# Optimization experiments

Hardware: AMD Instinct MI355X
Metric: run time of the kernel (lower is better)

## Reference

```python
import jax, jax.numpy as jnp
import numpy as np

D, H, L, P, NQ, B, DFF = 256, 8, 4, 4, 900, 4, 1024
SHAPES = [(128, 128), (64, 64), (32, 32), (16, 16)]
S = sum(h * w for h, w in SHAPES)  # 21760
HD = D // H


def setup_inputs() -> dict:
    key = jax.random.key(0)
    ks = iter(jax.random.split(key, 32))
    r = lambda sh, s=1.0: jax.random.normal(next(ks), sh, jnp.float32) * s
    return dict(
        tgt=r((B, NQ, D)),
        query_pos=r((B, NQ, D)),
        reference_points=jax.random.uniform(next(ks), (B, NQ, L, 2), jnp.float32),
        memory=r((B, S, D)),
        in_proj_w=r((D, 3 * D), 0.02), in_proj_b=jnp.zeros(3 * D, jnp.float32),
        out_proj_w=r((D, D), 0.02), out_proj_b=jnp.zeros(D, jnp.float32),
        ln1_g=jnp.ones(D, jnp.float32), ln1_b=jnp.zeros(D, jnp.float32),
        ln2_g=jnp.ones(D, jnp.float32), ln2_b=jnp.zeros(D, jnp.float32),
        ln3_g=jnp.ones(D, jnp.float32), ln3_b=jnp.zeros(D, jnp.float32),
        vproj_w=r((D, D), 0.02), vproj_b=jnp.zeros(D, jnp.float32),
        off_w=r((D, H * L * P * 2), 0.02), off_b=r((H * L * P * 2,), 0.5),
        aw_w=r((D, H * L * P), 0.02), aw_b=jnp.zeros(H * L * P, jnp.float32),
        oproj_w=r((D, D), 0.02), oproj_b=jnp.zeros(D, jnp.float32),
        lin1_w=r((D, DFF), 0.02), lin1_b=jnp.zeros(DFF, jnp.float32),
        lin2_w=r((DFF, D), 0.02), lin2_b=jnp.zeros(D, jnp.float32),
        spatial_shapes=np.array(SHAPES, np.int32),
        mem_mask=jnp.zeros((B, S), bool),
    )


def _ln(x, g, b):
    m = jnp.mean(x, -1, keepdims=True)
    v = jnp.mean((x - m) ** 2, -1, keepdims=True)
    return (x - m) * jax.lax.rsqrt(v + 1e-5) * g + b


def reference(tgt, query_pos, reference_points, memory,
              in_proj_w, in_proj_b, out_proj_w, out_proj_b,
              ln1_g, ln1_b, ln2_g, ln2_b, ln3_g, ln3_b,
              vproj_w, vproj_b, off_w, off_b, aw_w, aw_b, oproj_w, oproj_b,
              lin1_w, lin1_b, lin2_w, lin2_b, spatial_shapes, mem_mask):
    shapes = np.asarray(spatial_shapes)  # static level shapes

    # ---- self attention (nn.MultiheadAttention, q=k=tgt+pos, v=tgt) ----
    qp = tgt + query_pos
    q = qp @ in_proj_w[:, :D] + in_proj_b[:D]
    k = qp @ in_proj_w[:, D:2 * D] + in_proj_b[D:2 * D]
    v = tgt @ in_proj_w[:, 2 * D:] + in_proj_b[2 * D:]
    split = lambda x: x.reshape(B, NQ, H, HD).transpose(0, 2, 1, 3)
    qh, kh, vh = split(q), split(k), split(v)
    att = jax.nn.softmax(jnp.einsum('bhqd,bhkd->bhqk', qh, kh) / np.sqrt(HD).astype(np.float32), -1)
    sa = jnp.einsum('bhqk,bhkd->bhqd', att, vh).transpose(0, 2, 1, 3).reshape(B, NQ, D)
    tgt = _ln(tgt + sa @ out_proj_w + out_proj_b, ln2_g, ln2_b)

    # ---- MSDeformAttn cross attention ----
    query = tgt + query_pos
    value = memory @ vproj_w + vproj_b
    value = jnp.where(mem_mask[..., None], 0.0, value).reshape(B, S, H, HD)
    off = (query @ off_w + off_b).reshape(B, NQ, H, L, P, 2)
    aw = jax.nn.softmax((query @ aw_w + aw_b).reshape(B, NQ, H, L * P), -1).reshape(B, NQ, H, L, P)
    # offset normalizer is (W_l, H_l)
    normalizer = jnp.stack([jnp.asarray(shapes[:, 1]), jnp.asarray(shapes[:, 0])], -1).astype(jnp.float32)
    loc = reference_points[:, :, None, :, None, :] + off / normalizer[None, None, None, :, None, :]

    acc = jnp.zeros((B, NQ, H, HD), tgt.dtype)
    start = 0
    bidx = jnp.arange(B)[:, None, None, None]
    hidx = jnp.arange(H)[None, None, :, None]
    for l in range(L):
        Hl, Wl = int(shapes[l, 0]), int(shapes[l, 1])
        vf = value[:, start:start + Hl * Wl]  # [B, Hl*Wl, H, HD]
        # grid_sample align_corners=False, zero padding: pixel = loc*size - 0.5
        x = loc[:, :, :, l, :, 0] * Wl - 0.5  # [B,NQ,H,P]
        y = loc[:, :, :, l, :, 1] * Hl - 0.5
        x0 = jnp.floor(x); y0 = jnp.floor(y)
        wx = x - x0; wy = y - y0
        x0i = x0.astype(jnp.int32); y0i = y0.astype(jnp.int32)

        def gather(xi, yi):
            valid = (xi >= 0) & (xi < Wl) & (yi >= 0) & (yi < Hl)
            idx = jnp.clip(yi, 0, Hl - 1) * Wl + jnp.clip(xi, 0, Wl - 1)
            g = vf[bidx, idx, hidx]  # [B,NQ,H,P,HD]
            return jnp.where(valid[..., None], g, 0.0)

        samp = (gather(x0i, y0i) * ((1 - wx) * (1 - wy))[..., None]
                + gather(x0i + 1, y0i) * (wx * (1 - wy))[..., None]
                + gather(x0i, y0i + 1) * ((1 - wx) * wy)[..., None]
                + gather(x0i + 1, y0i + 1) * (wx * wy)[..., None])
        acc = acc + (samp * aw[:, :, :, l, :, None]).sum(3)
        start += Hl * Wl

    ca = acc.reshape(B, NQ, D) @ oproj_w + oproj_b
    tgt = _ln(tgt + ca, ln1_g, ln1_b)

    # ---- FFN ----
    ff = jax.nn.relu(tgt @ lin1_w + lin1_b) @ lin2_w + lin2_b
    return _ln(tgt + ff, ln3_g, ln3_b)
```

## Files before the change

### kernel.cpp

```cpp
#include <hip/hip_runtime.h>
#include <hip/hip_bf16.h>

typedef __attribute__((ext_vector_type(8))) short bf16x8;
typedef __attribute__((ext_vector_type(4))) short bf16x4;
typedef __attribute__((ext_vector_type(4))) float f32x4;

#define DEV static __device__ __forceinline__

constexpr int Bc = 4, NQc = 900, Hc = 8, Sc = 21760;
constexpr int M1 = Bc * NQc;
constexpr int NQT = (NQc + 63) / 64;

DEV short f2bf(float f) {
  union { __hip_bfloat16 h; short s; } u;
  u.h = __float2bfloat16(f);
  return u.s;
}
DEV float bf2f(short s) {
  union { short s; __hip_bfloat16 h; } u;
  u.s = s;
  return __bfloat162float(u.h);
}

DEV void pack_body(const float* W, short* Wt, int K, int N, int t) {
  int kq = K >> 2;
  int n = t / kq;
  int k4 = (t - n * kq) * 4;
  bf16x4 o;
  o[0] = f2bf(W[(size_t)(k4 + 0) * N + n]);
  o[1] = f2bf(W[(size_t)(k4 + 1) * N + n]);
  o[2] = f2bf(W[(size_t)(k4 + 2) * N + n]);
  o[3] = f2bf(W[(size_t)(k4 + 3) * N + n]);
  *(bf16x4*)&Wt[((size_t)(k4 >> 5) * N + n) * 32 + (k4 & 31)] = o;
}

__global__ __launch_bounds__(256) void pack_all_k(
    const float* w0, short* t0,
    const float* w1, short* t1,
    const float* w2, short* t2,
    const float* w3, short* t3,
    const float* w4, short* t4,
    const float* w5, short* t5) {
  int t = blockIdx.x * 256 + threadIdx.x;
  if (t < 49152) pack_body(w0, t0, 256, 768, t);
  else if (t < 65536) pack_body(w1, t1, 256, 256, t - 49152);
  else if (t < 81920) pack_body(w2, t2, 256, 256, t - 65536);
  else if (t < 98304) pack_body(w3, t3, 256, 256, t - 81920);
  else if (t < 163840) pack_body(w4, t4, 256, 1024, t - 98304);
  else pack_body(w5, t5, 1024, 256, t - 163840);
}

template <int MODE, int ACT>
__global__ __launch_bounds__(256) void gemmv_k(
    const float* __restrict__ A, const float* __restrict__ A2,
    const short* __restrict__ Wt, const float* __restrict__ bias,
    void* __restrict__ Cv, float* __restrict__ C2, int M, int N, int K,
    const unsigned char* __restrict__ rowmask, const float* __restrict__ g,
    const float* __restrict__ beta, const float* __restrict__ resid,
    const float* __restrict__ qpos, float* __restrict__ out2) {
  __shared__ short As[64 * 40];
  __shared__ short Ws[256 * 40];
  const int nb = N >> 8;
  const int mb = blockIdx.x / nb, bn = blockIdx.x - mb * nb;
  const int tid = threadIdx.x;
  const int lane = tid & 63, wave = tid >> 6;
  const int l16 = lane & 15, quad = lane >> 4;
  const int sr = tid >> 2, sk = (tid & 3) * 8;
  const int arow = mb * 64 + sr;
  const bool aval = arow < M;
  const bool useA2 = (MODE == 2) ? (bn < 2) : (A2 != nullptr);
  const float* ap = A + (size_t)arow * K + sk;
  const float* ap2 = A2 ? A2 + (size_t)arow * K + sk : A;
  const short* wp = Wt + (size_t)(bn * 256 + tid) * 32;
  const size_t wstep = (size_t)N * 32;

  f32x4 acc[4][4] = {};
  float4 a0, a1;
  bf16x8 w0, w1, w2, w3;

  if (aval) {
    a0 = *(const float4*)ap;
    a1 = *(const float4*)(ap + 4);
    if (useA2) {
      float4 b0 = *(const float4*)ap2, b1 = *(const float4*)(ap2 + 4);
      a0.x += b0.x; a0.y += b0.y; a0.z += b0.z; a0.w += b0.w;
      a1.x += b1.x; a1.y += b1.y; a1.z += b1.z; a1.w += b1.w;
    }
  } else {
    a0 = make_float4(0.f, 0.f, 0.f, 0.f);
    a1 = a0;
  }
  w0 = *(const bf16x8*)(wp + 0);
  w1 = *(const bf16x8*)(wp + 8);
  w2 = *(const bf16x8*)(wp + 16);
  w3 = *(const bf16x8*)(wp + 24);

  const int KT = K >> 5;
  for (int it = 0; it < KT; ++it) {
    {
      bf16x8 t;
      t[0] = f2bf(a0.x); t[1] = f2bf(a0.y); t[2] = f2bf(a0.z); t[3] = f2bf(a0.w);
      t[4] = f2bf(a1.x); t[5] = f2bf(a1.y); t[6] = f2bf(a1.z); t[7] = f2bf(a1.w);
      *(bf16x8*)&As[sr * 40 + sk] = t;
    }
    short* wd = &Ws[tid * 40];
    *(bf16x8*)(wd + 0) = w0;
    *(bf16x8*)(wd + 8) = w1;
    *(bf16x8*)(wd + 16) = w2;
    *(bf16x8*)(wd + 24) = w3;
    __syncthreads();
    if (it + 1 < KT) {
      const float* an = ap + (it + 1) * 32;
      if (aval) {
        a0 = *(const float4*)an;
        a1 = *(const float4*)(an + 4);
        if (useA2) {
          const float* an2 = ap2 + (it + 1) * 32;
          float4 b0 = *(const float4*)an2, b1 = *(const float4*)(an2 + 4);
          a0.x += b0.x; a0.y += b0.y; a0.z += b0.z; a0.w += b0.w;
          a1.x += b1.x; a1.y += b1.y; a1.z += b1.z; a1.w += b1.w;
        }
      }
      const short* wn = wp + (it + 1) * wstep;
      w0 = *(const bf16x8*)(wn + 0);
      w1 = *(const bf16x8*)(wn + 8);
      w2 = *(const bf16x8*)(wn + 16);
      w3 = *(const bf16x8*)(wn + 24);
    }
    bf16x8 af[4], bf[4];
#pragma unroll
    for (int i = 0; i < 4; i++)
      af[i] = *(const bf16x8*)&As[(i * 16 + l16) * 40 + quad * 8];
#pragma unroll
    for (int j = 0; j < 4; j++)
      bf[j] = *(const bf16x8*)&Ws[(wave * 64 + j * 16 + l16) * 40 + quad * 8];
#pragma unroll
    for (int i = 0; i < 4; i++)
#pragma unroll
      for (int j = 0; j < 4; j++)
        acc[i][j] = __builtin_amdgcn_mfma_f32_16x16x32_bf16(af[i], bf[j], acc[i][j], 0, 0, 0);
    __syncthreads();
  }

  if (MODE == 2) {
    const bool isqk = (bn < 2);
    float* dst = isqk ? (float*)Cv : C2;
    const int stride = isqk ? 512 : 256;
    const int cb = isqk ? bn * 256 : 0;
#pragma unroll
    for (int i = 0; i < 4; i++)
#pragma unroll
      for (int j = 0; j < 4; j++) {
        const int cl = wave * 64 + j * 16 + l16;
        const float bb = bias[bn * 256 + cl];
#pragma unroll
        for (int r = 0; r < 4; r++) {
          const int m = mb * 64 + i * 16 + quad * 4 + r;
          if (m < M) dst[(size_t)m * stride + cb + cl] = acc[i][j][r] + bb;
        }
      }
  } else if (MODE == 1) {
#pragma unroll
    for (int i = 0; i < 4; i++)
#pragma unroll
      for (int j = 0; j < 4; j++) {
        const int cl = wave * 64 + j * 16 + l16;
        const float bb = bias[cl];
#pragma unroll
        for (int r = 0; r < 4; r++) {
          const int m = mb * 64 + i * 16 + quad * 4 + r;
          if (m < M) {
            float v = acc[i][j][r] + bb;
            if (rowmask[m]) v = 0.f;
            ((short*)Cv)[(size_t)m * 256 + cl] = f2bf(v);
          }
        }
      }
  } else if (MODE == 0) {
#pragma unroll
    for (int i = 0; i < 4; i++)
#pragma unroll
      for (int j = 0; j < 4; j++) {
        const int cl = wave * 64 + j * 16 + l16;
        const int col = bn * 256 + cl;
        const float bb = bias[col];
#pragma unroll
        for (int r = 0; r < 4; r++) {
          const int m = mb * 64 + i * 16 + quad * 4 + r;
          if (m < M) {
            float v = acc[i][j][r] + bb;
            if (ACT == 1) v = fmaxf(v, 0.f);
            ((float*)Cv)[(size_t)m * N + col] = v;
          }
        }
      }
  } else {
#pragma unroll
    for (int j = 0; j < 4; j++) {
      const int cl = wave * 64 + j * 16 + l16;
      const float bb = bias[cl];
#pragma unroll
      for (int i = 0; i < 4; i++)
#pragma unroll
        for (int r = 0; r < 4; r++) {
          const int m = mb * 64 + i * 16 + quad * 4 + r;
          const float rs = (m < M) ? resid[(size_t)m * 256 + cl] : 0.f;
          acc[i][j][r] += bb + rs;
        }
    }
    float2* pr = (float2*)As;
#pragma unroll
    for (int i = 0; i < 4; i++)
#pragma unroll
      for (int r = 0; r < 4; r++) {
        float s = 0.f, q = 0.f;
#pragma unroll
        for (int j = 0; j < 4; j++) {
          s += acc[i][j][r];
          q += acc[i][j][r] * acc[i][j][r];
        }
#pragma unroll
        for (int d = 1; d < 16; d <<= 1) {
          s += __shfl_xor(s, d);
          q += __shfl_xor(q, d);
        }
        if (l16 == 0) pr[(i * 16 + quad * 4 + r) * 4 + wave] = make_float2(s, q);
      }
    __syncthreads();
#pragma unroll
    for (int i = 0; i < 4; i++)
#pragma unroll
      for (int r = 0; r < 4; r++) {
        const int ml = i * 16 + quad * 4 + r;
        float2 p0 = pr[ml * 4 + 0], p1 = pr[ml * 4 + 1];
        float2 p2 = pr[ml * 4 + 2], p3 = pr[ml * 4 + 3];
        const float sum = p0.x + p1.x + p2.x + p3.x;
        const float sq = p0.y + p1.y + p2.y + p3.y;
        const float mean = sum * (1.f / 256.f);
        const float var = sq * (1.f / 256.f) - mean * mean;
        const float rstd = rsqrtf(var + 1e-5f);
        const int m = mb * 64 + ml;
        if (m < M) {
#pragma unroll
          for (int j = 0; j < 4; j++) {
            const int cl = wave * 64 + j * 16 + l16;
            const float o = (acc[i][j][r] - mean) * rstd * g[cl] + beta[cl];
            ((float*)Cv)[(size_t)m * 256 + cl] = o;
            if (out2) out2[(size_t)m * 256 + cl] = o + qpos[(size_t)m * 256 + cl];
          }
        }
      }
  }
}

DEV void gemm32_body(const float* __restrict__ A, const float* __restrict__ W,
                     const float* __restrict__ bias, float* __restrict__ C,
                     int M, int N, int K, int bid) {
  __shared__ float Asf[16][64];
  __shared__ float Bsf[16][68];
  const int nb = N >> 6;
  const int bm = bid / nb, bn = bid % nb;
  const int tid = threadIdx.x;
  const int tm = tid >> 4, tn = tid & 15;
  float acc[4][4] = {};

  for (int k0 = 0; k0 < K; k0 += 16) {
    {
      const int m = tid >> 2, kk = (tid & 3) * 4;
      const int row = bm * 64 + m;
      float4 v = (row < M) ? *(const float4*)(A + (size_t)row * K + k0 + kk)
                           : make_float4(0.f, 0.f, 0.f, 0.f);
      Asf[kk + 0][m] = v.x; Asf[kk + 1][m] = v.y;
      Asf[kk + 2][m] = v.z; Asf[kk + 3][m] = v.w;
    }
    {
      const int kk = tid >> 4, n = (tid & 15) * 4;
      float4 v = *(const float4*)(W + (size_t)(k0 + kk) * N + bn * 64 + n);
      *(float4*)&Bsf[kk][n] = v;
    }
    __syncthreads();
#pragma unroll
    for (int kk = 0; kk < 16; kk++) {
      float a[4], b[4];
#pragma unroll
      for (int i = 0; i < 4; i++) a[i] = Asf[kk][tm * 4 + i];
#pragma unroll
      for (int j = 0; j < 4; j++) b[j] = Bsf[kk][tn * 4 + j];
#pragma unroll
      for (int i = 0; i < 4; i++)
#pragma unroll
        for (int j = 0; j < 4; j++) acc[i][j] = fmaf(a[i], b[j], acc[i][j]);
    }
    __syncthreads();
  }
#pragma unroll
  for (int i = 0; i < 4; i++) {
    const int row = bm * 64 + tm * 4 + i;
    if (row >= M) continue;
#pragma unroll
    for (int j = 0; j < 4; j++) {
      const int col = bn * 64 + tn * 4 + j;
      C[(size_t)row * N + col] = acc[i][j] + bias[col];
    }
  }
}

__global__ __launch_bounds__(256) void gemm32_offaw_k(
    const float* __restrict__ query, const float* __restrict__ off_w,
    const float* __restrict__ off_b, float* __restrict__ offb,
    const float* __restrict__ aw_w, const float* __restrict__ aw_b,
    float* __restrict__ awlin) {
  if (blockIdx.x < 228)
    gemm32_body(query, off_w, off_b, offb, M1, 256, 256, blockIdx.x);
  else
    gemm32_body(query, aw_w, aw_b, awlin, M1, 128, 256, blockIdx.x - 228);
}

__global__ __launch_bounds__(256) void attn_k(const float* __restrict__ qk,
                                              const float* __restrict__ vbuf,
                                              float* __restrict__ sa) {
  __shared__ short Vt[32 * 72];
  __shared__ short Pb[4][16 * 72];
  const int bid = blockIdx.x;
  const int qt = bid % NQT, bh = bid / NQT;
  const int b = bh >> 3, h = bh & 7;
  const int tid = threadIdx.x, lane = tid & 63, wave = tid >> 6;
  const int l16 = lane & 15, quad = lane >> 4;

  const int q_local = qt * 64 + wave * 16 + l16;
  const int qrow = b * NQc + min(q_local, NQc - 1);
  const float scale = 0.17677669529663687f;
  bf16x8 qf;
  {
    const float* qp = qk + (size_t)qrow * 512 + h * 32 + quad * 8;
    float4 v0 = *(const float4*)qp, v1 = *(const float4*)(qp + 4);
    qf[0] = f2bf(v0.x * scale); qf[1] = f2bf(v0.y * scale);
    qf[2] = f2bf(v0.z * scale); qf[3] = f2bf(v0.w * scale);
    qf[4] = f2bf(v1.x * scale); qf[5] = f2bf(v1.y * scale);
    qf[6] = f2bf(v1.z * scale); qf[7] = f2bf(v1.w * scale);
  }
  f32x4 o0 = {}, o1 = {};
  float mrun[4] = {-1e30f, -1e30f, -1e30f, -1e30f};
  float lrun[4] = {0.f, 0.f, 0.f, 0.f};

  for (int kt = 0; kt < NQT; kt++) {
    const int k0 = kt * 64;
    __syncthreads();
#pragma unroll
    for (int i = 0; i < 8; i++) {
      int kk = i * 8 + (tid >> 5);
      int ch = tid & 31;
      int key = k0 + kk;
      float v = (key < NQc) ? vbuf[(size_t)(b * NQc + key) * 256 + h * 32 + ch] : 0.f;
      Vt[ch * 72 + kk] = f2bf(v);
    }
    __syncthreads();

    f32x4 s[4];
#pragma unroll
    for (int st = 0; st < 4; st++) {
      const int key = k0 + st * 16 + l16;
      const int krow = b * NQc + min(key, NQc - 1);
      const float* kp = qk + (size_t)krow * 512 + 256 + h * 32 + quad * 8;
      float4 v0 = *(const float4*)kp, v1 = *(const float4*)(kp + 4);
      bf16x8 kf;
      kf[0] = f2bf(v0.x); kf[1] = f2bf(v0.y); kf[2] = f2bf(v0.z); kf[3] = f2bf(v0.w);
      kf[4] = f2bf(v1.x); kf[5] = f2bf(v1.y); kf[6] = f2bf(v1.z); kf[7] = f2bf(v1.w);
      f32x4 z = {};
      s[st] = __builtin_amdgcn_mfma_f32_16x16x32_bf16(qf, kf, z, 0, 0, 0);
      if (key >= NQc) { s[st][0] = -1e30f; s[st][1] = -1e30f; s[st][2] = -1e30f; s[st][3] = -1e30f; }
    }
    float mnew[4], alpha[4];
#pragma unroll
    for (int r = 0; r < 4; r++) {
      float mx = fmaxf(fmaxf(s[0][r], s[1][r]), fmaxf(s[2][r], s[3][r]));
#pragma unroll
      for (int d = 1; d < 16; d <<= 1) mx = fmaxf(mx, __shfl_xor(mx, d));
      mnew[r] = fmaxf(mrun[r], mx);
      alpha[r] = __expf(mrun[r] - mnew[r]);
      mrun[r] = mnew[r];
    }
    float tsum[4] = {0.f, 0.f, 0.f, 0.f};
#pragma unroll
    for (int st = 0; st < 4; st++) {
#pragma unroll
      for (int r = 0; r < 4; r++) {
        float p = __expf(s[st][r] - mnew[r]);
        s[st][r] = p;
        tsum[r] += p;
      }
    }
#pragma unroll
    for (int r = 0; r < 4; r++) {
      float t = tsum[r];
#pragma unroll
      for (int d = 1; d < 16; d <<= 1) t += __shfl_xor(t, d);
      lrun[r] = lrun[r] * alpha[r] + t;
      o0[r] *= alpha[r];
      o1[r] *= alpha[r];
    }
    short* pw = Pb[wave];
#pragma unroll
    for (int st = 0; st < 4; st++)
#pragma unroll
      for (int r = 0; r < 4; r++)
        pw[(quad * 4 + r) * 72 + st * 16 + l16] = f2bf(s[st][r]);
#pragma unroll
    for (int c = 0; c < 2; c++) {
      bf16x8 pf = *(const bf16x8*)&pw[l16 * 72 + c * 32 + quad * 8];
      bf16x8 vf0 = *(const bf16x8*)&Vt[l16 * 72 + c * 32 + quad * 8];
      bf16x8 vf1 = *(const bf16x8*)&Vt[(16 + l16) * 72 + c * 32 + quad * 8];
      o0 = __builtin_amdgcn_mfma_f32_16x16x32_bf16(pf, vf0, o0, 0, 0, 0);
      o1 = __builtin_amdgcn_mfma_f32_16x16x32_bf16(pf, vf1, o1, 0, 0, 0);
    }
  }
#pragma unroll
  for (int r = 0; r < 4; r++) {
    const int q = qt * 64 + wave * 16 + quad * 4 + r;
    if (q < NQc) {
      const float inv = 1.f / lrun[r];
      sa[(size_t)(b * NQc + q) * 256 + h * 32 + l16] = o0[r] * inv;
      sa[(size_t)(b * NQc + q) * 256 + h * 32 + 16 + l16] = o1[r] * inv;
    }
  }
}

__global__ __launch_bounds__(256) void sample_k(
    const float* __restrict__ awlin, const float* __restrict__ off,
    const float* __restrict__ refp, const short* __restrict__ value,
    float* __restrict__ accout) {
  const int wid = blockIdx.x * 4 + (threadIdx.x >> 6);
  const int lane = threadIdx.x & 63;
  const int bq = wid >> 3, h = wid & 7;
  const int b = bq / NQc;
  const int l16 = lane & 15;

  float wraw = awlin[(size_t)bq * 128 + h * 16 + l16];
  float mx = wraw;
#pragma unroll
  for (int d = 1; d < 16; d <<= 1) mx = fmaxf(mx, __shfl_xor(mx, d));
  float e = __expf(wraw - mx), ssum = e;
#pragma unroll
  for (int d = 1; d < 16; d <<= 1) ssum += __shfl_xor(ssum, d);
  const float wnorm = e / ssum;

  const int ch = lane & 31, sub = lane >> 5;
  float facc = 0.f;
#pragma unroll
  for (int it = 0; it < 8; it++) {
    const int pt = it * 2 + sub;
    const float w = __shfl(wnorm, pt);
    const int l = pt >> 2;
    const int W = 128 >> l;
    const int start = (l == 0) ? 0 : (l == 1) ? 16384 : (l == 2) ? 20480 : 21504;
    const float offx = off[(size_t)bq * 256 + h * 32 + pt * 2];
    const float offy = off[(size_t)bq * 256 + h * 32 + pt * 2 + 1];
    const float rx = refp[(size_t)bq * 8 + l * 2];
    const float ry = refp[(size_t)bq * 8 + l * 2 + 1];
    const float x = rx * (float)W + offx - 0.5f;
    const float y = ry * (float)W + offy - 0.5f;
    const float x0f = floorf(x), y0f = floorf(y);
    const float wx = x - x0f, wy = y - y0f;
    const int x0 = (int)x0f, y0 = (int)y0f;
    const short* vb = value + ((size_t)b * Sc + start) * 256 + h * 32 + ch;
#pragma unroll
    for (int c4 = 0; c4 < 4; c4++) {
      const int dx = c4 & 1, dy = c4 >> 1;
      const int xi = x0 + dx, yi = y0 + dy;
      const bool valid = (xi >= 0) && (xi < W) && (yi >= 0) && (yi < W);
      const int xc = min(max(xi, 0), W - 1);
      const int yc = min(max(yi, 0), W - 1);
      const float gvv = bf2f(vb[(size_t)(yc * W + xc) * 256]);
      const float ww = (dx ? wx : 1.f - wx) * (dy ? wy : 1.f - wy);
      facc += valid ? w * ww * gvv : 0.f;
    }
  }
  facc += __shfl_xor(facc, 32);
  if (lane < 32) accout[(size_t)bq * 256 + h * 32 + ch] = facc;
}

extern "C" void kernel_launch(void* const* d_in, const int* in_sizes, int n_in,
                              void* d_out, int out_size, void* d_ws,
                              size_t ws_size, hipStream_t stream) {
  const float* tgt = (const float*)d_in[0];
  const float* query_pos = (const float*)d_in[1];
  const float* refp = (const float*)d_in[2];
  const float* memory = (const float*)d_in[3];
  const float* in_proj_w = (const float*)d_in[4];
  const float* in_proj_b = (const float*)d_in[5];
  const float* out_proj_w = (const float*)d_in[6];
  const float* out_proj_b = (const float*)d_in[7];
  const float* ln1_g = (const float*)d_in[8];
  const float* ln1_b = (const float*)d_in[9];
  const float* ln2_g = (const float*)d_in[10];
  const float* ln2_b = (const float*)d_in[11];
  const float* ln3_g = (const float*)d_in[12];
  const float* ln3_b = (const float*)d_in[13];
  const float* vproj_w = (const float*)d_in[14];
  const float* vproj_b = (const float*)d_in[15];
  const float* off_w = (const float*)d_in[16];
  const float* off_b = (const float*)d_in[17];
  const float* aw_w = (const float*)d_in[18];
  const float* aw_b = (const float*)d_in[19];
  const float* oproj_w = (const float*)d_in[20];
  const float* oproj_b = (const float*)d_in[21];
  const float* lin1_w = (const float*)d_in[22];
  const float* lin1_b = (const float*)d_in[23];
  const float* lin2_w = (const float*)d_in[24];
  const float* lin2_b = (const float*)d_in[25];
  const unsigned char* mem_mask = (const unsigned char*)d_in[27];
  float* out = (float*)d_out;

  float* ws = (float*)d_ws;
  float* qkbuf = ws + 921600;
  float* vbuf = ws + 2764800;
  float* sa = ws + 3686400;
  float* tgt2 = ws + 5529600;
  float* query = ws + 6451200;
  float* offb = ws + 7372800;
  float* awlin = ws + 8294400;
  float* accb = ws + 8755200;
  float* tgt3 = ws + 9676800;
  float* ff1 = ws + 10598400;
  short* valueBf = (short*)(ws + 14284800);
  short* wbase = valueBf + 22282240;
  short* inT = wbase + 0;
  short* outT = wbase + 196608;
  short* vT = wbase + 262144;
  short* oT = wbase + 327680;
  short* lin1T = wbase + 393216;
  short* lin2T = wbase + 655360;

  pack_all_k<<<896, 256, 0, stream>>>(in_proj_w, inT, out_proj_w, outT,
                                      vproj_w, vT, oproj_w, oT,
                                      lin1_w, lin1T, lin2_w, lin2T);

  gemmv_k<2, 0><<<57 * 3, 256, 0, stream>>>(
      tgt, query_pos, inT, in_proj_b, qkbuf, vbuf, M1, 768, 256,
      nullptr, nullptr, nullptr, nullptr, nullptr, nullptr);
  attn_k<<<Bc * Hc * NQT, 256, 0, stream>>>(qkbuf, vbuf, sa);
  gemmv_k<3, 0><<<57, 256, 0, stream>>>(
      sa, nullptr, outT, out_proj_b, tgt2, nullptr, M1, 256, 256,
      nullptr, ln2_g, ln2_b, tgt, query_pos, query);
  gemmv_k<1, 0><<<1360, 256, 0, stream>>>(
      memory, nullptr, vT, vproj_b, valueBf, nullptr, Bc * Sc, 256, 256,
      mem_mask, nullptr, nullptr, nullptr, nullptr, nullptr);
  gemm32_offaw_k<<<342, 256, 0, stream>>>(query, off_w, off_b, offb, aw_w, aw_b, awlin);
  sample_k<<<Bc * NQc * Hc / 4, 256, 0, stream>>>(awlin, offb, refp, valueBf, accb);
  gemmv_k<3, 0><<<57, 256, 0, stream>>>(
      accb, nullptr, oT, oproj_b, tgt3, nullptr, M1, 256, 256,
      nullptr, ln1_g, ln1_b, tgt2, nullptr, nullptr);
  gemmv_k<0, 1><<<57 * 4, 256, 0, stream>>>(
      tgt3, nullptr, lin1T, lin1_b, ff1, nullptr, M1, 1024, 256,
      nullptr, nullptr, nullptr, nullptr, nullptr, nullptr);
  gemmv_k<3, 0><<<57, 256, 0, stream>>>(
      ff1, nullptr, lin2T, lin2_b, out, nullptr, M1, 256, 1024,
      nullptr, ln3_g, ln3_b, tgt3, nullptr, nullptr);
}
```

Measured before the change: 487.1 us.

## Split attention keys across waves and shrink GEMM row tiles for more blocks

Self-attention now gives each block 16 queries and splits the key tiles across its 4 waves. Each wave keeps a private V tile, and the partial softmax states are merged through shared memory at the end. This removes the per-tile block barriers and launches four times as many blocks. The small-M GEMMs gain a 32-row tile variant with a two-stage register double-buffered load loop, and the weight pack kernel's index mapping is changed so consecutive threads read coalesced columns. The risks are more redundant V loads per block and extra barriers in the GEMM loop.

```diff
diff --git a/kernel.cpp b/kernel.cpp
--- a/kernel.cpp
+++ b/kernel.cpp
@@ -10,6 +10,7 @@
 constexpr int Bc = 4, NQc = 900, Hc = 8, Sc = 21760;
 constexpr int M1 = Bc * NQc;
 constexpr int NQT = (NQc + 63) / 64;
+constexpr int QT16 = (NQc + 15) / 16;
 
 DEV short f2bf(float f) {
   union { __hip_bfloat16 h; short s; } u;
@@ -23,9 +24,8 @@
 }
 
 DEV void pack_body(const float* W, short* Wt, int K, int N, int t) {
-  int kq = K >> 2;
-  int n = t / kq;
-  int k4 = (t - n * kq) * 4;
+  int n = t % N;
+  int k4 = (t / N) * 4;
   bf16x4 o;
   o[0] = f2bf(W[(size_t)(k4 + 0) * N + n]);
   o[1] = f2bf(W[(size_t)(k4 + 1) * N + n]);
@@ -35,12 +35,9 @@
 }
 
 __global__ __launch_bounds__(256) void pack_all_k(
-    const float* w0, short* t0,
-    const float* w1, short* t1,
-    const float* w2, short* t2,
-    const float* w3, short* t3,
-    const float* w4, short* t4,
-    const float* w5, short* t5) {
+    const float* w0, short* t0, const float* w1, short* t1,
+    const float* w2, short* t2, const float* w3, short* t3,
+    const float* w4, short* t4, const float* w5, short* t5) {
   int t = blockIdx.x * 256 + threadIdx.x;
   if (t < 49152) pack_body(w0, t0, 256, 768, t);
   else if (t < 65536) pack_body(w1, t1, 256, 256, t - 49152);
@@ -50,7 +47,7 @@
   else pack_body(w5, t5, 1024, 256, t - 163840);
 }
 
-template <int MODE, int ACT>
+template <int MODE, int ACT, int MT>
 __global__ __launch_bounds__(256) void gemmv_k(
     const float* __restrict__ A, const float* __restrict__ A2,
     const short* __restrict__ Wt, const float* __restrict__ bias,
@@ -58,117 +55,126 @@
     const unsigned char* __restrict__ rowmask, const float* __restrict__ g,
     const float* __restrict__ beta, const float* __restrict__ resid,
     const float* __restrict__ qpos, float* __restrict__ out2) {
-  __shared__ short As[64 * 40];
+  constexpr int IT = MT / 16;
+  __shared__ short As[MT * 40];
   __shared__ short Ws[256 * 40];
   const int nb = N >> 8;
   const int mb = blockIdx.x / nb, bn = blockIdx.x - mb * nb;
   const int tid = threadIdx.x;
   const int lane = tid & 63, wave = tid >> 6;
   const int l16 = lane & 15, quad = lane >> 4;
-  const int sr = tid >> 2, sk = (tid & 3) * 8;
-  const int arow = mb * 64 + sr;
+  const int sr = (MT == 64) ? (tid >> 2) : (tid >> 3);
+  const int sk = (MT == 64) ? ((tid & 3) * 8) : ((tid & 7) * 4);
+  const int arow = mb * MT + sr;
   const bool aval = arow < M;
   const bool useA2 = (MODE == 2) ? (bn < 2) : (A2 != nullptr);
   const float* ap = A + (size_t)arow * K + sk;
-  const float* ap2 = A2 ? A2 + (size_t)arow * K + sk : A;
+  const float* ap2 = (A2 ? A2 : A) + (size_t)arow * K + sk;
   const short* wp = Wt + (size_t)(bn * 256 + tid) * 32;
   const size_t wstep = (size_t)N * 32;
-
-  f32x4 acc[4][4] = {};
-  float4 a0, a1;
-  bf16x8 w0, w1, w2, w3;
-
-  if (aval) {
-    a0 = *(const float4*)ap;
-    a1 = *(const float4*)(ap + 4);
-    if (useA2) {
-      float4 b0 = *(const float4*)ap2, b1 = *(const float4*)(ap2 + 4);
-      a0.x += b0.x; a0.y += b0.y; a0.z += b0.z; a0.w += b0.w;
-      a1.x += b1.x; a1.y += b1.y; a1.z += b1.z; a1.w += b1.w;
-    }
-  } else {
-    a0 = make_float4(0.f, 0.f, 0.f, 0.f);
-    a1 = a0;
-  }
-  w0 = *(const bf16x8*)(wp + 0);
-  w1 = *(const bf16x8*)(wp + 8);
-  w2 = *(const bf16x8*)(wp + 16);
-  w3 = *(const bf16x8*)(wp + 24);
-
   const int KT = K >> 5;
-  for (int it = 0; it < KT; ++it) {
-    {
+
+  f32x4 acc[IT][4] = {};
+  float4 pa0[2] = {}, pa1[2] = {};
+  bf16x8 pw[2][4];
+
+  auto loadA = [&](int s, int it) {
+    if (aval) {
+      const float* p = ap + it * 32;
+      pa0[s] = *(const float4*)p;
+      if constexpr (MT == 64) pa1[s] = *(const float4*)(p + 4);
+      if (useA2) {
+        const float* p2 = ap2 + it * 32;
+        float4 q0 = *(const float4*)p2;
+        pa0[s].x += q0.x; pa0[s].y += q0.y; pa0[s].z += q0.z; pa0[s].w += q0.w;
+        if constexpr (MT == 64) {
+          float4 q1 = *(const float4*)(p2 + 4);
+          pa1[s].x += q1.x; pa1[s].y += q1.y; pa1[s].z += q1.z; pa1[s].w += q1.w;
+        }
+      }
+    }
+  };
+  auto loadW = [&](int s, int it) {
+    const short* p = wp + (size_t)it * wstep;
+    pw[s][0] = *(const bf16x8*)(p + 0);
+    pw[s][1] = *(const bf16x8*)(p + 8);
+    pw[s][2] = *(const bf16x8*)(p + 16);
+    pw[s][3] = *(const bf16x8*)(p + 24);
+  };
+  auto stage = [&](int s) {
+    if constexpr (MT == 64) {
       bf16x8 t;
-      t[0] = f2bf(a0.x); t[1] = f2bf(a0.y); t[2] = f2bf(a0.z); t[3] = f2bf(a0.w);
-      t[4] = f2bf(a1.x); t[5] = f2bf(a1.y); t[6] = f2bf(a1.z); t[7] = f2bf(a1.w);
+      t[0] = f2bf(pa0[s].x); t[1] = f2bf(pa0[s].y); t[2] = f2bf(pa0[s].z); t[3] = f2bf(pa0[s].w);
+      t[4] = f2bf(pa1[s].x); t[5] = f2bf(pa1[s].y); t[6] = f2bf(pa1[s].z); t[7] = f2bf(pa1[s].w);
       *(bf16x8*)&As[sr * 40 + sk] = t;
+    } else {
+      bf16x4 t;
+      t[0] = f2bf(pa0[s].x); t[1] = f2bf(pa0[s].y); t[2] = f2bf(pa0[s].z); t[3] = f2bf(pa0[s].w);
+      *(bf16x4*)&As[sr * 40 + sk] = t;
     }
     short* wd = &Ws[tid * 40];
-    *(bf16x8*)(wd + 0) = w0;
-    *(bf16x8*)(wd + 8) = w1;
-    *(bf16x8*)(wd + 16) = w2;
-    *(bf16x8*)(wd + 24) = w3;
-    __syncthreads();
-    if (it + 1 < KT) {
-      const float* an = ap + (it + 1) * 32;
-      if (aval) {
-        a0 = *(const float4*)an;
-        a1 = *(const float4*)(an + 4);
-        if (useA2) {
-          const float* an2 = ap2 + (it + 1) * 32;
-          float4 b0 = *(const float4*)an2, b1 = *(const float4*)(an2 + 4);
-          a0.x += b0.x; a0.y += b0.y; a0.z += b0.z; a0.w += b0.w;
-          a1.x += b1.x; a1.y += b1.y; a1.z += b1.z; a1.w += b1.w;
-        }
-      }
-      const short* wn = wp + (it + 1) * wstep;
-      w0 = *(const bf16x8*)(wn + 0);
-      w1 = *(const bf16x8*)(wn + 8);
-      w2 = *(const bf16x8*)(wn + 16);
-      w3 = *(const bf16x8*)(wn + 24);
-    }
-    bf16x8 af[4], bf[4];
-#pragma unroll
-    for (int i = 0; i < 4; i++)
+    *(bf16x8*)(wd + 0) = pw[s][0];
+    *(bf16x8*)(wd + 8) = pw[s][1];
+    *(bf16x8*)(wd + 16) = pw[s][2];
+    *(bf16x8*)(wd + 24) = pw[s][3];
+  };
+  auto compute = [&]() {
+    bf16x8 af[IT], bfr[4];
+#pragma unroll
+    for (int i = 0; i < IT; i++)
       af[i] = *(const bf16x8*)&As[(i * 16 + l16) * 40 + quad * 8];
 #pragma unroll
     for (int j = 0; j < 4; j++)
-      bf[j] = *(const bf16x8*)&Ws[(wave * 64 + j * 16 + l16) * 40 + quad * 8];
-#pragma unroll
-    for (int i = 0; i < 4; i++)
+      bfr[j] = *(const bf16x8*)&Ws[(wave * 64 + j * 16 + l16) * 40 + quad * 8];
+#pragma unroll
+    for (int i = 0; i < IT; i++)
 #pragma unroll
       for (int j = 0; j < 4; j++)
-        acc[i][j] = __builtin_amdgcn_mfma_f32_16x16x32_bf16(af[i], bf[j], acc[i][j], 0, 0, 0);
-    __syncthreads();
-  }
-
-  if (MODE == 2) {
+        acc[i][j] = __builtin_amdgcn_mfma_f32_16x16x32_bf16(af[i], bfr[j], acc[i][j], 0, 0, 0);
+  };
+
+  loadA(0, 0); loadW(0, 0);
+  loadA(1, 1); loadW(1, 1);
+  for (int it = 0; it < KT; it += 2) {
+    stage(0);
+    __syncthreads();
+    if (it + 2 < KT) { loadA(0, it + 2); loadW(0, it + 2); }
+    compute();
+    __syncthreads();
+    stage(1);
+    __syncthreads();
+    if (it + 3 < KT) { loadA(1, it + 3); loadW(1, it + 3); }
+    compute();
+    __syncthreads();
+  }
+
+  if constexpr (MODE == 2) {
     const bool isqk = (bn < 2);
     float* dst = isqk ? (float*)Cv : C2;
     const int stride = isqk ? 512 : 256;
     const int cb = isqk ? bn * 256 : 0;
 #pragma unroll
-    for (int i = 0; i < 4; i++)
+    for (int i = 0; i < IT; i++)
 #pragma unroll
       for (int j = 0; j < 4; j++) {
         const int cl = wave * 64 + j * 16 + l16;
         const float bb = bias[bn * 256 + cl];
 #pragma unroll
         for (int r = 0; r < 4; r++) {
-          const int m = mb * 64 + i * 16 + quad * 4 + r;
+          const int m = mb * MT + i * 16 + quad * 4 + r;
           if (m < M) dst[(size_t)m * stride + cb + cl] = acc[i][j][r] + bb;
         }
       }
-  } else if (MODE == 1) {
-#pragma unroll
-    for (int i = 0; i < 4; i++)
+  } else if constexpr (MODE == 1) {
+#pragma unroll
+    for (int i = 0; i < IT; i++)
 #pragma unroll
       for (int j = 0; j < 4; j++) {
         const int cl = wave * 64 + j * 16 + l16;
         const float bb = bias[cl];
 #pragma unroll
         for (int r = 0; r < 4; r++) {
-          const int m = mb * 64 + i * 16 + quad * 4 + r;
+          const int m = mb * MT + i * 16 + quad * 4 + r;
           if (m < M) {
             float v = acc[i][j][r] + bb;
             if (rowmask[m]) v = 0.f;
@@ -176,9 +182,9 @@
           }
         }
       }
-  } else if (MODE == 0) {
-#pragma unroll
-    for (int i = 0; i < 4; i++)
+  } else if constexpr (MODE == 0) {
+#pragma unroll
+    for (int i = 0; i < IT; i++)
 #pragma unroll
       for (int j = 0; j < 4; j++) {
         const int cl = wave * 64 + j * 16 + l16;
@@ -186,7 +192,7 @@
         const float bb = bias[col];
 #pragma unroll
         for (int r = 0; r < 4; r++) {
-          const int m = mb * 64 + i * 16 + quad * 4 + r;
+          const int m = mb * MT + i * 16 + quad * 4 + r;
           if (m < M) {
             float v = acc[i][j][r] + bb;
             if (ACT == 1) v = fmaxf(v, 0.f);
@@ -200,17 +206,17 @@
       const int cl = wave * 64 + j * 16 + l16;
       const float bb = bias[cl];
 #pragma unroll
-      for (int i = 0; i < 4; i++)
+      for (int i = 0; i < IT; i++)
 #pragma unroll
         for (int r = 0; r < 4; r++) {
-          const int m = mb * 64 + i * 16 + quad * 4 + r;
+          const int m = mb * MT + i * 16 + quad * 4 + r;
           const float rs = (m < M) ? resid[(size_t)m * 256 + cl] : 0.f;
           acc[i][j][r] += bb + rs;
         }
     }
     float2* pr = (float2*)As;
 #pragma unroll
-    for (int i = 0; i < 4; i++)
+    for (int i = 0; i < IT; i++)
 #pragma unroll
       for (int r = 0; r < 4; r++) {
         float s = 0.f, q = 0.f;
@@ -228,7 +234,7 @@
       }
     __syncthreads();
 #pragma unroll
-    for (int i = 0; i < 4; i++)
+    for (int i = 0; i < IT; i++)
 #pragma unroll
       for (int r = 0; r < 4; r++) {
         const int ml = i * 16 + quad * 4 + r;
@@ -239,7 +245,7 @@
         const float mean = sum * (1.f / 256.f);
         const float var = sq * (1.f / 256.f) - mean * mean;
         const float rstd = rsqrtf(var + 1e-5f);
-        const int m = mb * 64 + ml;
+        const int m = mb * MT + ml;
         if (m < M) {
 #pragma unroll
           for (int j = 0; j < 4; j++) {
@@ -319,15 +325,17 @@
 __global__ __launch_bounds__(256) void attn_k(const float* __restrict__ qk,
                                               const float* __restrict__ vbuf,
                                               float* __restrict__ sa) {
-  __shared__ short Vt[32 * 72];
+  __shared__ short Vt[4][32 * 72];
   __shared__ short Pb[4][16 * 72];
+  __shared__ float Om[4][16][32];
+  __shared__ float Ml[4][16][2];
   const int bid = blockIdx.x;
-  const int qt = bid % NQT, bh = bid / NQT;
+  const int qt = bid % QT16, bh = bid / QT16;
   const int b = bh >> 3, h = bh & 7;
   const int tid = threadIdx.x, lane = tid & 63, wave = tid >> 6;
   const int l16 = lane & 15, quad = lane >> 4;
 
-  const int q_local = qt * 64 + wave * 16 + l16;
+  const int q_local = qt * 16 + l16;
   const int qrow = b * NQc + min(q_local, NQc - 1);
   const float scale = 0.17677669529663687f;
   bf16x8 qf;
@@ -343,19 +351,18 @@
   float mrun[4] = {-1e30f, -1e30f, -1e30f, -1e30f};
   float lrun[4] = {0.f, 0.f, 0.f, 0.f};
 
-  for (int kt = 0; kt < NQT; kt++) {
+  short* vt = Vt[wave];
+  short* pw = Pb[wave];
+  const int vch = lane & 31, vkk = lane >> 5;
+
+  for (int kt = wave; kt < NQT; kt += 4) {
     const int k0 = kt * 64;
-    __syncthreads();
-#pragma unroll
-    for (int i = 0; i < 8; i++) {
-      int kk = i * 8 + (tid >> 5);
-      int ch = tid & 31;
-      int key = k0 + kk;
-      float v = (key < NQc) ? vbuf[(size_t)(b * NQc + key) * 256 + h * 32 + ch] : 0.f;
-      Vt[ch * 72 + kk] = f2bf(v);
-    }
-    __syncthreads();
-
+#pragma unroll
+    for (int i = 0; i < 32; i++) {
+      const int key = k0 + 2 * i + vkk;
+      const float v = (key < NQc) ? vbuf[(size_t)(b * NQc + key) * 256 + h * 32 + vch] : 0.f;
+      vt[vch * 72 + 2 * i + vkk] = f2bf(v);
+    }
     f32x4 s[4];
 #pragma unroll
     for (int st = 0; st < 4; st++) {
@@ -382,14 +389,13 @@
     }
     float tsum[4] = {0.f, 0.f, 0.f, 0.f};
 #pragma unroll
-    for (int st = 0; st < 4; st++) {
+    for (int st = 0; st < 4; st++)
 #pragma unroll
       for (int r = 0; r < 4; r++) {
         float p = __expf(s[st][r] - mnew[r]);
         s[st][r] = p;
         tsum[r] += p;
       }
-    }
 #pragma unroll
     for (int r = 0; r < 4; r++) {
       float t = tsum[r];
@@ -399,7 +405,6 @@
       o0[r] *= alpha[r];
       o1[r] *= alpha[r];
     }
-    short* pw = Pb[wave];
 #pragma unroll
     for (int st = 0; st < 4; st++)
 #pragma unroll
@@ -408,19 +413,45 @@
 #pragma unroll
     for (int c = 0; c < 2; c++) {
       bf16x8 pf = *(const bf16x8*)&pw[l16 * 72 + c * 32 + quad * 8];
-      bf16x8 vf0 = *(const bf16x8*)&Vt[l16 * 72 + c * 32 + quad * 8];
-      bf16x8 vf1 = *(const bf16x8*)&Vt[(16 + l16) * 72 + c * 32 + quad * 8];
+      bf16x8 vf0 = *(const bf16x8*)&vt[l16 * 72 + c * 32 + quad * 8];
+      bf16x8 vf1 = *(const bf16x8*)&vt[(16 + l16) * 72 + c * 32 + quad * 8];
       o0 = __builtin_amdgcn_mfma_f32_16x16x32_bf16(pf, vf0, o0, 0, 0, 0);
       o1 = __builtin_amdgcn_mfma_f32_16x16x32_bf16(pf, vf1, o1, 0, 0, 0);
     }
   }
 #pragma unroll
   for (int r = 0; r < 4; r++) {
-    const int q = qt * 64 + wave * 16 + quad * 4 + r;
-    if (q < NQc) {
-      const float inv = 1.f / lrun[r];
-      sa[(size_t)(b * NQc + q) * 256 + h * 32 + l16] = o0[r] * inv;
-      sa[(size_t)(b * NQc + q) * 256 + h * 32 + 16 + l16] = o1[r] * inv;
+    Om[wave][quad * 4 + r][l16] = o0[r];
+    Om[wave][quad * 4 + r][16 + l16] = o1[r];
+  }
+  if (l16 == 0) {
+#pragma unroll
+    for (int r = 0; r < 4; r++) {
+      Ml[wave][quad * 4 + r][0] = mrun[r];
+      Ml[wave][quad * 4 + r][1] = lrun[r];
+    }
+  }
+  __syncthreads();
+  {
+    const int q = tid >> 4;
+    const int c2 = (tid & 15) * 2;
+    const float m0 = Ml[0][q][0], m1 = Ml[1][q][0];
+    const float m2 = Ml[2][q][0], m3 = Ml[3][q][0];
+    const float M = fmaxf(fmaxf(m0, m1), fmaxf(m2, m3));
+    const float a0 = __expf(m0 - M), a1 = __expf(m1 - M);
+    const float a2 = __expf(m2 - M), a3 = __expf(m3 - M);
+    const float lsum = a0 * Ml[0][q][1] + a1 * Ml[1][q][1] +
+                       a2 * Ml[2][q][1] + a3 * Ml[3][q][1];
+    const float s0 = a0 * Om[0][q][c2] + a1 * Om[1][q][c2] +
+                     a2 * Om[2][q][c2] + a3 * Om[3][q][c2];
+    const float s1 = a0 * Om[0][q][c2 + 1] + a1 * Om[1][q][c2 + 1] +
+                     a2 * Om[2][q][c2 + 1] + a3 * Om[3][q][c2 + 1];
+    const int qg = qt * 16 + q;
+    if (qg < NQc) {
+      const float inv = 1.f / lsum;
+      float* dst = sa + ((size_t)(b * NQc + qg) * 256 + h * 32 + c2);
+      dst[0] = s0 * inv;
+      dst[1] = s1 * inv;
     }
   }
 }
@@ -535,25 +566,25 @@
                                       vproj_w, vT, oproj_w, oT,
                                       lin1_w, lin1T, lin2_w, lin2T);
 
-  gemmv_k<2, 0><<<57 * 3, 256, 0, stream>>>(
+  gemmv_k<2, 0, 32><<<113 * 3, 256, 0, stream>>>(
       tgt, query_pos, inT, in_proj_b, qkbuf, vbuf, M1, 768, 256,
       nullptr, nullptr, nullptr, nullptr, nullptr, nullptr);
-  attn_k<<<Bc * Hc * NQT, 256, 0, stream>>>(qkbuf, vbuf, sa);
-  gemmv_k<3, 0><<<57, 256, 0, stream>>>(
+  attn_k<<<Bc * Hc * QT16, 256, 0, stream>>>(qkbuf, vbuf, sa);
+  gemmv_k<3, 0, 32><<<113, 256, 0, stream>>>(
       sa, nullptr, outT, out_proj_b, tgt2, nullptr, M1, 256, 256,
       nullptr, ln2_g, ln2_b, tgt, query_pos, query);
-  gemmv_k<1, 0><<<1360, 256, 0, stream>>>(
+  gemmv_k<1, 0, 64><<<1360, 256, 0, stream>>>(
       memory, nullptr, vT, vproj_b, valueBf, nullptr, Bc * Sc, 256, 256,
       mem_mask, nullptr, nullptr, nullptr, nullptr, nullptr);
   gemm32_offaw_k<<<342, 256, 0, stream>>>(query, off_w, off_b, offb, aw_w, aw_b, awlin);
   sample_k<<<Bc * NQc * Hc / 4, 256, 0, stream>>>(awlin, offb, refp, valueBf, accb);
-  gemmv_k<3, 0><<<57, 256, 0, stream>>>(
+  gemmv_k<3, 0, 32><<<113, 256, 0, stream>>>(
       accb, nullptr, oT, oproj_b, tgt3, nullptr, M1, 256, 256,
       nullptr, ln1_g, ln1_b, tgt2, nullptr, nullptr);
-  gemmv_k<0, 1><<<57 * 4, 256, 0, stream>>>(
+  gemmv_k<0, 1, 64><<<57 * 4, 256, 0, stream>>>(
       tgt3, nullptr, lin1T, lin1_b, ff1, nullptr, M1, 1024, 256,
       nullptr, nullptr, nullptr, nullptr, nullptr, nullptr);
-  gemmv_k<3, 0><<<57, 256, 0, stream>>>(
+  gemmv_k<3, 0, 32><<<113, 256, 0, stream>>>(
       ff1, nullptr, lin2T, lin2_b, out, nullptr, M1, 256, 1024,
       nullptr, ln3_g, ln3_b, tgt3, nullptr, nullptr);
 }
```

Measured after the change: 470.4 us. -3.4%, faster.
